# Kernel tuning notes

Hardware: AMD Instinct MI355X
Metric: run time of the kernel (lower is better)

## Reference

```python
import jax, jax.numpy as jnp
import numpy as np

T, B, E = 512, 128, 256  # timesteps, batch_size, embedding_size


def setup_inputs() -> dict:
    key = jax.random.key(0)
    k1, k2, k3 = jax.random.split(key, 3)
    return {
        "v": jax.random.normal(k1, (T, B, E), dtype=jnp.float32),
        "u": jax.random.uniform(k2, (T, B), dtype=jnp.float32),  # pop signals in (0,1)
        "d": jax.random.uniform(k3, (T, B), dtype=jnp.float32),  # push signals in (0,1)
    }


def _pop(s, w):
    """Grefenstette-stack pop: s [T,B] strengths (stack grows along dim 0,
    padded with zeros past the current depth), w [B] pop amount.
    Reverse cumsum, subtract w, clamp at 0, then difference to recover per-slot
    strengths. Zero padding at the tail is preserved exactly (contributes 0)."""
    top = jnp.cumsum(s[::-1], axis=0) - w[None, :]
    top = jnp.clip(top, 0.0)
    top = top - jnp.concatenate([jnp.zeros_like(top[:1]), top[:-1]], axis=0)
    return top[::-1]


def reference(v, u, d):
    # v: [T, B, E] pushed vectors; u, d: [T, B] pop/push strengths.
    T_, B_ = u.shape
    E_ = v.shape[-1]
    ones = jnp.ones((B_,), v.dtype)

    def step(carry, xs):
        V, s = carry  # V: [T,B,E] value buffer, s: [T,B] strengths (zero-padded)
        t, v_t, u_t, d_t = xs
        V = V.at[t].set(v_t)
        # forward(): pop with u (original detaches s and u inside pop), then push d
        s = _pop(jax.lax.stop_gradient(s), jax.lax.stop_gradient(u_t)).at[t].set(d_t)
        # read(): weights = s - pop(s, 1); r = sum_t weights * V
        weights = s - _pop(jax.lax.stop_gradient(s), ones)
        r = jnp.einsum('tb,tbe->be', weights, V)
        return (V, s), r

    init = (jnp.zeros((T_, B_, E_), v.dtype), jnp.zeros((T_, B_), v.dtype))
    _, rs = jax.lax.scan(step, init, (jnp.arange(T_), v, u, d))
    return rs  # [T, B, E] read vector at each timestep
```

## Files before the change

kernel.cpp:

```cpp
#include <hip/hip_runtime.h>

#define T_DIM 512
#define B_DIM 128
#define E_DIM 256
#define NEG_INF (-1e30f)

typedef float vfloat4 __attribute__((ext_vector_type(4)));


struct Node { float g; int ngl; };

__global__ void __launch_bounds__(512) scan_prep(
    const float* __restrict__ u, const float* __restrict__ d,
    float* __restrict__ S_out, Node* __restrict__ nodes)
{
    const int b    = blockIdx.x;
    const int t    = threadIdx.x;
    const int lane = t & 63;
    const int w    = t >> 6;

    __shared__ float wsum[8];
    __shared__ float wpre[8];
    __shared__ float M[10][T_DIM];

    const float dv = d[t * B_DIM + b];
    float x = dv - u[t * B_DIM + b];

    #pragma unroll
    for (int off = 1; off < 64; off <<= 1) {
        float y = __shfl_up(x, off, 64);
        if (lane >= off) x += y;
    }
    if (lane == 63) wsum[w] = x;
    __syncthreads();
    if (t < 8) {
        float s = 0.f;
        for (int i = 0; i < t; ++i) s += wsum[i];
        wpre[t] = s;
    }
    __syncthreads();
    const float S = x + wpre[w];
    const float g = dv - S;

    M[0][t] = g;
    __syncthreads();
    #pragma unroll
    for (int k = 1; k < 10; ++k) {
        int h = 1 << (k - 1);
        float left = (t >= h) ? M[k - 1][t - h] : NEG_INF;
        float mk = fmaxf(M[k - 1][t], left);
        __syncthreads();
        M[k][t] = mk;
        __syncthreads();
    }

    int m = t - 1;
    #pragma unroll
    for (int k = 9; k >= 0; --k) {
        if (m >= 0 && M[k][m] <= g) m -= (1 << k);
    }
    if (m < 0) m = -1;

    S_out[(b << 9) | t] = S;
    nodes[(b << 9) | t] = Node{g, m};
}

#define CPW 4
__global__ void __launch_bounds__(256) stack_read(
    const float* __restrict__ v, const float* __restrict__ S_in,
    const Node* __restrict__ nodes, float* __restrict__ out)
{
    const int wid  = (blockIdx.x << 2) | (threadIdx.x >> 6);
    const int lane = threadIdx.x & 63;
    const int e4   = lane << 2;

    float4 acc[CPW];
    float  prev[CPW], Sv[CPW];
    int    m[CPW], bb[CPW];
    bool   act[CPW];

    #pragma unroll
    for (int c = 0; c < CPW; ++c) {
        const int id = (wid << 2) | c;
        bb[c]  = id >> 9;
        m[c]   = id & 511;
        Sv[c]  = S_in[id];
        acc[c] = make_float4(0.f, 0.f, 0.f, 0.f);
        prev[c] = 0.f;
        act[c]  = true;
    }

    while (act[0] || act[1] || act[2] || act[3]) {
        Node  nd[CPW];
        float4 vv[CPW];
        #pragma unroll
        for (int c = 0; c < CPW; ++c) {
            if (act[c]) {
                nd[c] = nodes[(bb[c] << 9) | m[c]];
                vv[c] = *(const float4*)(v + ((size_t)m[c] * B_DIM + bb[c]) * E_DIM + e4);
            }
        }
        #pragma unroll
        for (int c = 0; c < CPW; ++c) {
            if (act[c]) {
                const float rc  = Sv[c] + nd[c].g;
                const float cur = fminf(rc, 1.f);
                const float wt  = cur - prev[c];
                acc[c].x += wt * vv[c].x;
                acc[c].y += wt * vv[c].y;
                acc[c].z += wt * vv[c].z;
                acc[c].w += wt * vv[c].w;
                prev[c] = cur;
                if (rc >= 1.f || nd[c].ngl < 0) act[c] = false;
                else                            m[c] = nd[c].ngl;
            }
        }
    }

    #pragma unroll
    for (int c = 0; c < CPW; ++c) {
        const int id = (wid << 2) | c;
        vfloat4 val = {acc[c].x, acc[c].y, acc[c].z, acc[c].w};
        vfloat4* o = (vfloat4*)(out + ((size_t)(id & 511) * B_DIM + (id >> 9)) * E_DIM + e4);
        __builtin_nontemporal_store(val, o);
    }
}

extern "C" void kernel_launch(void* const* d_in, const int* in_sizes, int n_in,
                              void* d_out, int out_size, void* d_ws, size_t ws_size,
                              hipStream_t stream) {
    const float* v = (const float*)d_in[0];
    const float* u = (const float*)d_in[1];
    const float* d = (const float*)d_in[2];
    float* out = (float*)d_out;

    float* S    = (float*)d_ws;
    Node*  node = (Node*)((char*)d_ws + (size_t)B_DIM * T_DIM * 4);

    scan_prep<<<dim3(B_DIM), 512, 0, stream>>>(u, d, S, node);
    stack_read<<<dim3((T_DIM * B_DIM) / (CPW * 4)), 256, 0, stream>>>(v, S, node, out);
}
```

Before: 137.8 us.

## Stage per-batch time windows of v in LDS and share chain walks

Each block now handles a 32-timestep window for one batch element. It loads that window's v rows, nodes and S into shared memory, plus up to 16 earlier chain rows found by walking back from the window start. Per-timestep read chains are then served from LDS first and fall back to global memory only past the cached prefix. This aims to cut redundant global gathers of the same v rows across neighbouring timesteps. The cost is extra shared memory, a serial single-lane prefix walk, and less parallel latency hiding than the previous 4-chain interleave.

```diff
diff --git a/kernel.cpp b/kernel.cpp
--- a/kernel.cpp
+++ b/kernel.cpp
@@ -4,6 +4,8 @@
 #define B_DIM 128
 #define E_DIM 256
 #define NEG_INF (-1e30f)
+#define W_WIN 32
+#define L_SLOTS 16
 
 typedef float vfloat4 __attribute__((ext_vector_type(4)));
 
@@ -65,64 +67,119 @@
     nodes[(b << 9) | t] = Node{g, m};
 }
 
-#define CPW 4
 __global__ void __launch_bounds__(256) stack_read(
     const float* __restrict__ v, const float* __restrict__ S_in,
     const Node* __restrict__ nodes, float* __restrict__ out)
 {
-    const int wid  = (blockIdx.x << 2) | (threadIdx.x >> 6);
-    const int lane = threadIdx.x & 63;
-    const int e4   = lane << 2;
+    __shared__ float vwin[W_WIN][E_DIM];
+    __shared__ float vL[L_SLOTS][E_DIM];
+    __shared__ float wg_g[W_WIN];
+    __shared__ int   wg_ngl[W_WIN];
+    __shared__ float wg_S[W_WIN];
+    __shared__ int   Lidx[L_SLOTS];
+    __shared__ float Lg[L_SLOTS];
+    __shared__ int   Lcount, Lnext;
 
-    float4 acc[CPW];
-    float  prev[CPW], Sv[CPW];
-    int    m[CPW], bb[CPW];
-    bool   act[CPW];
+    const int b     = blockIdx.x >> 4;
+    const int t0    = (blockIdx.x & 15) << 5;
+    const int tid   = threadIdx.x;
+    const int w     = tid >> 6;
+    const int lane  = tid & 63;
+    const int e4    = lane << 2;
+    const int nbase = b << 9;
 
-    #pragma unroll
-    for (int c = 0; c < CPW; ++c) {
-        const int id = (wid << 2) | c;
-        bb[c]  = id >> 9;
-        m[c]   = id & 511;
-        Sv[c]  = S_in[id];
-        acc[c] = make_float4(0.f, 0.f, 0.f, 0.f);
-        prev[c] = 0.f;
-        act[c]  = true;
+    if (w == 0) {
+        float sv = 1e30f;
+        if (lane < W_WIN) {
+            const int t = t0 + lane;
+            sv = S_in[nbase | t];
+            const Node nd = nodes[nbase | t];
+            wg_S[lane]   = sv;
+            wg_g[lane]   = nd.g;
+            wg_ngl[lane] = nd.ngl;
+        }
+        #pragma unroll
+        for (int off = 32; off; off >>= 1) sv = fminf(sv, __shfl_xor(sv, off, 64));
+        if (lane == 0) {
+            const float smin = sv;
+            int lc = 0, m = t0 - 1, mn = -1;
+            while (m >= 0 && lc < L_SLOTS) {
+                const Node nd = nodes[nbase | m];
+                Lidx[lc] = m; Lg[lc] = nd.g; ++lc;
+                mn = nd.ngl;
+                if (nd.g >= 1.0f - smin) break;
+                m = nd.ngl;
+            }
+            Lcount = lc; Lnext = mn;
+        }
     }
+    for (int r = w; r < W_WIN; r += 4) {
+        const float4 x = *(const float4*)(v + ((size_t)(t0 + r) * B_DIM + b) * E_DIM + e4);
+        *(float4*)&vwin[r][e4] = x;
+    }
+    __syncthreads();
+    const int lc = Lcount;
+    for (int r = w; r < lc; r += 4) {
+        const int m = Lidx[r];
+        const float4 x = *(const float4*)(v + ((size_t)m * B_DIM + b) * E_DIM + e4);
+        *(float4*)&vL[r][e4] = x;
+    }
+    __syncthreads();
+    const int lnx = Lnext;
 
-    while (act[0] || act[1] || act[2] || act[3]) {
-        Node  nd[CPW];
-        float4 vv[CPW];
-        #pragma unroll
-        for (int c = 0; c < CPW; ++c) {
-            if (act[c]) {
-                nd[c] = nodes[(bb[c] << 9) | m[c]];
-                vv[c] = *(const float4*)(v + ((size_t)m[c] * B_DIM + bb[c]) * E_DIM + e4);
+    for (int j = 0; j < 8; ++j) {
+        const int tw = (w << 3) | j;
+        const int t  = t0 + tw;
+        const float S = wg_S[tw];
+        float4 acc = make_float4(0.f, 0.f, 0.f, 0.f);
+        float prev = 0.f;
+        int m = t;
+        bool active = true;
+
+        while (active && m >= t0) {
+            const int k = m - t0;
+            const float g  = wg_g[k];
+            const float rc = S + g;
+            const float cur = fminf(rc, 1.f);
+            const float wt  = cur - prev; prev = cur;
+            const float4 vv = *(const float4*)&vwin[k][e4];
+            acc.x += wt * vv.x; acc.y += wt * vv.y;
+            acc.z += wt * vv.z; acc.w += wt * vv.w;
+            if (rc >= 1.f) { active = false; break; }
+            m = wg_ngl[k];
+            if (m < 0) active = false;
+        }
+        if (active && m >= 0) {
+            int i = 0;
+            while (i < lc && Lidx[i] != m) ++i;
+            if (i < lc) {
+                for (; i < lc; ++i) {
+                    const float g  = Lg[i];
+                    const float rc = S + g;
+                    const float cur = fminf(rc, 1.f);
+                    const float wt  = cur - prev; prev = cur;
+                    const float4 vv = *(const float4*)&vL[i][e4];
+                    acc.x += wt * vv.x; acc.y += wt * vv.y;
+                    acc.z += wt * vv.z; acc.w += wt * vv.w;
+                    if (rc >= 1.f) { active = false; break; }
+                }
+                if (active) m = lnx;
+            }
+            while (active && m >= 0) {
+                const Node nd = nodes[nbase | m];
+                const float rc = S + nd.g;
+                const float cur = fminf(rc, 1.f);
+                const float wt  = cur - prev; prev = cur;
+                const float4 vv = *(const float4*)(v + ((size_t)m * B_DIM + b) * E_DIM + e4);
+                acc.x += wt * vv.x; acc.y += wt * vv.y;
+                acc.z += wt * vv.z; acc.w += wt * vv.w;
+                if (rc >= 1.f) break;
+                m = nd.ngl;
             }
         }
-        #pragma unroll
-        for (int c = 0; c < CPW; ++c) {
-            if (act[c]) {
-                const float rc  = Sv[c] + nd[c].g;
-                const float cur = fminf(rc, 1.f);
-                const float wt  = cur - prev[c];
-                acc[c].x += wt * vv[c].x;
-                acc[c].y += wt * vv[c].y;
-                acc[c].z += wt * vv[c].z;
-                acc[c].w += wt * vv[c].w;
-                prev[c] = cur;
-                if (rc >= 1.f || nd[c].ngl < 0) act[c] = false;
-                else                            m[c] = nd[c].ngl;
-            }
-        }
-    }
-
-    #pragma unroll
-    for (int c = 0; c < CPW; ++c) {
-        const int id = (wid << 2) | c;
-        vfloat4 val = {acc[c].x, acc[c].y, acc[c].z, acc[c].w};
-        vfloat4* o = (vfloat4*)(out + ((size_t)(id & 511) * B_DIM + (id >> 9)) * E_DIM + e4);
-        __builtin_nontemporal_store(val, o);
+        const vfloat4 val = {acc.x, acc.y, acc.z, acc.w};
+        __builtin_nontemporal_store(val,
+            (vfloat4*)(out + ((size_t)t * B_DIM + b) * E_DIM + e4));
     }
 }
 
@@ -138,5 +195,5 @@
     Node*  node = (Node*)((char*)d_ws + (size_t)B_DIM * T_DIM * 4);
 
     scan_prep<<<dim3(B_DIM), 512, 0, stream>>>(u, d, S, node);
-    stack_read<<<dim3((T_DIM * B_DIM) / (CPW * 4)), 256, 0, stream>>>(v, S, node, out);
+    stack_read<<<dim3((T_DIM / W_WIN) * B_DIM), 256, 0, stream>>>(v, S, node, out);
 }
```

Result: slower. 151.4 us (+9.9%).

## Precompute per-query gather lists in scan kernel and batch independent vector loads

Applied to the files above, without the earlier changes.

The scan kernel now walks each query's chain of stack slots, capped at a fixed length, and writes the weights and slot indices into a per-query list in workspace. The read kernel reads these lists in chunks of four and issues four independent vector loads per chunk, instead of a dependent pointer-chase through node records for every step. Chains longer than the cap fall back to the old traversal. The change also swizzles block order and gives each wave two queries instead of four. In exchange it adds 256 bytes of list storage per query and moves serial chain walking into the prep kernel, which runs with only one block per batch element.

```diff
diff --git a/kernel.cpp b/kernel.cpp
--- a/kernel.cpp
+++ b/kernel.cpp
@@ -4,15 +4,17 @@
 #define B_DIM 128
 #define E_DIM 256
 #define NEG_INF (-1e30f)
+#define CAP 28
 
 typedef float vfloat4 __attribute__((ext_vector_type(4)));
 
 
 struct Node { float g; int ngl; };
 
+
 __global__ void __launch_bounds__(512) scan_prep(
     const float* __restrict__ u, const float* __restrict__ d,
-    float* __restrict__ S_out, Node* __restrict__ nodes)
+    float* __restrict__ lists, Node* __restrict__ nodes)
 {
     const int b    = blockIdx.x;
     const int t    = threadIdx.x;
@@ -22,6 +24,7 @@
     __shared__ float wsum[8];
     __shared__ float wpre[8];
     __shared__ float M[10][T_DIM];
+    __shared__ int   sngl[T_DIM];
 
     const float dv = d[t * B_DIM + b];
     float x = dv - u[t * B_DIM + b];
@@ -61,68 +64,101 @@
     }
     if (m < 0) m = -1;
 
-    S_out[(b << 9) | t] = S;
-    nodes[(b << 9) | t] = Node{g, m};
+    const int id = (b << 9) | t;
+    nodes[id] = Node{g, m};
+    sngl[t] = m;
+    __syncthreads();
+
+    float* Lb = lists + (size_t)id * 64;
+    float prev = 0.f;
+    int   cm = t, cnt = 0, cont_m = -1;
+    float cont_prev = 0.f;
+    while (true) {
+        const float gm = M[0][cm];
+        const float rc = S + gm;
+        const float cur = fminf(rc, 1.f);
+        Lb[4 + 2 * cnt] = cur - prev;
+        Lb[5 + 2 * cnt] = __int_as_float(cm);
+        prev = cur;
+        ++cnt;
+        if (rc >= 1.f) break;
+        const int nm = sngl[cm];
+        if (nm < 0) break;
+        cm = nm;
+        if (cnt == CAP) { cont_m = cm; cont_prev = prev; break; }
+    }
+    const int last_m = cm;
+    while (cnt & 3) {
+        Lb[4 + 2 * cnt] = 0.f;
+        Lb[5 + 2 * cnt] = __int_as_float(last_m);
+        ++cnt;
+    }
+    Lb[0] = __int_as_float(cnt);
+    Lb[1] = __int_as_float(cont_m);
+    Lb[2] = cont_prev;
+    Lb[3] = S;
 }
 
-#define CPW 4
-__global__ void __launch_bounds__(256) stack_read(
-    const float* __restrict__ v, const float* __restrict__ S_in,
+__global__ void __launch_bounds__(256) gather_read(
+    const float* __restrict__ v, const float* __restrict__ lists,
     const Node* __restrict__ nodes, float* __restrict__ out)
 {
-    const int wid  = (blockIdx.x << 2) | (threadIdx.x >> 6);
+    const int bid  = blockIdx.x;
+    const int swz  = ((bid & 7) << 10) | (bid >> 3);
+    const int wid  = (swz << 2) | (threadIdx.x >> 6);
     const int lane = threadIdx.x & 63;
     const int e4   = lane << 2;
 
-    float4 acc[CPW];
-    float  prev[CPW], Sv[CPW];
-    int    m[CPW], bb[CPW];
-    bool   act[CPW];
+    #pragma unroll
+    for (int c = 0; c < 2; ++c) {
+        const int id = (wid << 1) | c;
+        const int b  = id >> 9, t = id & 511;
+        const float* __restrict__ vb = v + (size_t)b * E_DIM + e4;
+        const float4* __restrict__ Lb = (const float4*)(lists + (size_t)id * 64);
 
-    #pragma unroll
-    for (int c = 0; c < CPW; ++c) {
-        const int id = (wid << 2) | c;
-        bb[c]  = id >> 9;
-        m[c]   = id & 511;
-        Sv[c]  = S_in[id];
-        acc[c] = make_float4(0.f, 0.f, 0.f, 0.f);
-        prev[c] = 0.f;
-        act[c]  = true;
-    }
+        const float4 hdr = Lb[0];
+        const int cnt    = __float_as_int(hdr.x);
+        const int cont_m = __float_as_int(hdr.y);
+        const int nch    = cnt >> 2;
 
-    while (act[0] || act[1] || act[2] || act[3]) {
-        Node  nd[CPW];
-        float4 vv[CPW];
-        #pragma unroll
-        for (int c = 0; c < CPW; ++c) {
-            if (act[c]) {
-                nd[c] = nodes[(bb[c] << 9) | m[c]];
-                vv[c] = *(const float4*)(v + ((size_t)m[c] * B_DIM + bb[c]) * E_DIM + e4);
+        float4 acc = make_float4(0.f, 0.f, 0.f, 0.f);
+        for (int ch = 0; ch < nch; ++ch) {
+            const float4 q0 = Lb[1 + 2 * ch];
+            const float4 q1 = Lb[2 + 2 * ch];
+            const int ma = __float_as_int(q0.y);
+            const int mb = __float_as_int(q0.w);
+            const int mc = __float_as_int(q1.y);
+            const int md = __float_as_int(q1.w);
+            const float4 va = *(const float4*)(vb + ((size_t)ma << 15));
+            const float4 vc2 = *(const float4*)(vb + ((size_t)mb << 15));
+            const float4 vc3 = *(const float4*)(vb + ((size_t)mc << 15));
+            const float4 vc4 = *(const float4*)(vb + ((size_t)md << 15));
+            acc.x += q0.x * va.x + q0.z * vc2.x + q1.x * vc3.x + q1.z * vc4.x;
+            acc.y += q0.x * va.y + q0.z * vc2.y + q1.x * vc3.y + q1.z * vc4.y;
+            acc.z += q0.x * va.z + q0.z * vc2.z + q1.x * vc3.z + q1.z * vc4.z;
+            acc.w += q0.x * va.w + q0.z * vc2.w + q1.x * vc3.w + q1.z * vc4.w;
+        }
+
+        if (cont_m >= 0) {
+            float prev = hdr.z;
+            const float S = hdr.w;
+            int m = cont_m;
+            while (m >= 0) {
+                const Node nd = nodes[(b << 9) | m];
+                const float rc = S + nd.g;
+                const float cur = fminf(rc, 1.f);
+                const float wt = cur - prev; prev = cur;
+                const float4 vv = *(const float4*)(vb + ((size_t)m << 15));
+                acc.x += wt * vv.x; acc.y += wt * vv.y;
+                acc.z += wt * vv.z; acc.w += wt * vv.w;
+                if (rc >= 1.f) break;
+                m = nd.ngl;
             }
         }
-        #pragma unroll
-        for (int c = 0; c < CPW; ++c) {
-            if (act[c]) {
-                const float rc  = Sv[c] + nd[c].g;
-                const float cur = fminf(rc, 1.f);
-                const float wt  = cur - prev[c];
-                acc[c].x += wt * vv[c].x;
-                acc[c].y += wt * vv[c].y;
-                acc[c].z += wt * vv[c].z;
-                acc[c].w += wt * vv[c].w;
-                prev[c] = cur;
-                if (rc >= 1.f || nd[c].ngl < 0) act[c] = false;
-                else                            m[c] = nd[c].ngl;
-            }
-        }
-    }
 
-    #pragma unroll
-    for (int c = 0; c < CPW; ++c) {
-        const int id = (wid << 2) | c;
-        vfloat4 val = {acc[c].x, acc[c].y, acc[c].z, acc[c].w};
-        vfloat4* o = (vfloat4*)(out + ((size_t)(id & 511) * B_DIM + (id >> 9)) * E_DIM + e4);
-        __builtin_nontemporal_store(val, o);
+        const vfloat4 val = {acc.x, acc.y, acc.z, acc.w};
+        __builtin_nontemporal_store(val,
+            (vfloat4*)(out + ((size_t)t * B_DIM + b) * E_DIM + e4));
     }
 }
 
@@ -134,9 +170,9 @@
     const float* d = (const float*)d_in[2];
     float* out = (float*)d_out;
 
-    float* S    = (float*)d_ws;
-    Node*  node = (Node*)((char*)d_ws + (size_t)B_DIM * T_DIM * 4);
+    Node*  node  = (Node*)d_ws;
+    float* lists = (float*)((char*)d_ws + ((size_t)1 << 20));
 
-    scan_prep<<<dim3(B_DIM), 512, 0, stream>>>(u, d, S, node);
-    stack_read<<<dim3((T_DIM * B_DIM) / (CPW * 4)), 256, 0, stream>>>(v, S, node, out);
+    scan_prep<<<dim3(B_DIM), 512, 0, stream>>>(u, d, lists, node);
+    gather_read<<<dim3((T_DIM * B_DIM) / 8), 256, 0, stream>>>(v, lists, node, out);
 }
```

New measurement: 141.7 us. 2.8% more time.

## Share chain traversal across 8 consecutive timesteps per wave with LDS-cached nodes

Applied to the files above, without the earlier changes.

Each wave now handles 8 consecutive timesteps of one batch column rather than 4 unrelated ones. They walk a merged greater-previous chain, so every loaded v row is reused across all 8 outputs, and a running max threshold decides which outputs take each element. The batch's node table is staged into shared memory and block ids are swizzled for locality. This aims to cut redundant global loads of v and of the nodes, in exchange for more per-element compare logic and a shared-memory staging step.

```diff
diff --git a/kernel.cpp b/kernel.cpp
--- a/kernel.cpp
+++ b/kernel.cpp
@@ -4,6 +4,8 @@
 #define B_DIM 128
 #define E_DIM 256
 #define NEG_INF (-1e30f)
+#define W 8
+#define DONE 1e30f
 
 typedef float vfloat4 __attribute__((ext_vector_type(4)));
 
@@ -65,64 +67,109 @@
     nodes[(b << 9) | t] = Node{g, m};
 }
 
-#define CPW 4
 __global__ void __launch_bounds__(256) stack_read(
     const float* __restrict__ v, const float* __restrict__ S_in,
     const Node* __restrict__ nodes, float* __restrict__ out)
 {
-    const int wid  = (blockIdx.x << 2) | (threadIdx.x >> 6);
+    __shared__ float2 snode[T_DIM];
+
+    const int bid = blockIdx.x;
+    const int swz = ((bid & 7) << 8) | (bid >> 3);
+    const int base_id = swz << 5;
+    const int b    = base_id >> 9;
+    const int wv   = threadIdx.x >> 6;
     const int lane = threadIdx.x & 63;
     const int e4   = lane << 2;
 
-    float4 acc[CPW];
-    float  prev[CPW], Sv[CPW];
-    int    m[CPW], bb[CPW];
-    bool   act[CPW];
+    {
+        const int i = threadIdx.x;
+        const Node n0 = nodes[(b << 9) | i];
+        const Node n1 = nodes[(b << 9) | (i + 256)];
+        snode[i]       = make_float2(n0.g, __int_as_float(n0.ngl));
+        snode[i + 256] = make_float2(n1.g, __int_as_float(n1.ngl));
+    }
+    __syncthreads();
+
+    const int tw = (base_id & 511) | (wv << 3);
+    const float* __restrict__ vb = v + (size_t)b * E_DIM + e4;
+
+    float4 acc[W];
+    float  M[W], prev[W], S[W];
+    #pragma unroll
+    for (int j = 0; j < W; ++j) {
+        acc[j] = make_float4(0.f, 0.f, 0.f, 0.f);
+        M[j] = NEG_INF; prev[j] = 0.f;
+        S[j] = S_in[base_id + (wv << 3) + j];
+    }
 
     #pragma unroll
-    for (int c = 0; c < CPW; ++c) {
-        const int id = (wid << 2) | c;
-        bb[c]  = id >> 9;
-        m[c]   = id & 511;
-        Sv[c]  = S_in[id];
-        acc[c] = make_float4(0.f, 0.f, 0.f, 0.f);
-        prev[c] = 0.f;
-        act[c]  = true;
+    for (int k = W - 1; k >= 0; --k) {
+        const int m = tw + k;
+        const float2 nd = snode[m];
+        const float g = nd.x;
+        const float4 vv = *(const float4*)(vb + ((size_t)m << 15));
+        #pragma unroll
+        for (int j = 0; j < W; ++j) {
+            if (j >= k) {
+                if (g > M[j]) {
+                    const float rc  = S[j] + g;
+                    const float cur = fminf(rc, 1.f);
+                    const float wt  = cur - prev[j];
+                    acc[j].x += wt * vv.x; acc[j].y += wt * vv.y;
+                    acc[j].z += wt * vv.z; acc[j].w += wt * vv.w;
+                    prev[j] = cur;
+                    M[j] = (rc >= 1.f) ? DONE : g;
+                }
+            }
+        }
     }
 
-    while (act[0] || act[1] || act[2] || act[3]) {
-        Node  nd[CPW];
-        float4 vv[CPW];
-        #pragma unroll
-        for (int c = 0; c < CPW; ++c) {
-            if (act[c]) {
-                nd[c] = nodes[(bb[c] << 9) | m[c]];
-                vv[c] = *(const float4*)(v + ((size_t)m[c] * B_DIM + bb[c]) * E_DIM + e4);
+    float thr = M[0];
+    #pragma unroll
+    for (int j = 1; j < W; ++j) thr = fminf(thr, M[j]);
+
+    if (thr < 1e29f) {
+        int p = __float_as_int(snode[tw].y);
+        while (p >= 0) {
+            const float2 nd = snode[p];
+            if (nd.x > thr) break;
+            p = __float_as_int(nd.y);
+        }
+        while (p >= 0) {
+            const float2 nd = snode[p];
+            const float g = nd.x;
+            const float4 vv = *(const float4*)(vb + ((size_t)p << 15));
+            #pragma unroll
+            for (int j = 0; j < W; ++j) {
+                if (g > M[j]) {
+                    const float rc  = S[j] + g;
+                    const float cur = fminf(rc, 1.f);
+                    const float wt  = cur - prev[j];
+                    acc[j].x += wt * vv.x; acc[j].y += wt * vv.y;
+                    acc[j].z += wt * vv.z; acc[j].w += wt * vv.w;
+                    prev[j] = cur;
+                    M[j] = (rc >= 1.f) ? DONE : g;
+                }
             }
-        }
-        #pragma unroll
-        for (int c = 0; c < CPW; ++c) {
-            if (act[c]) {
-                const float rc  = Sv[c] + nd[c].g;
-                const float cur = fminf(rc, 1.f);
-                const float wt  = cur - prev[c];
-                acc[c].x += wt * vv[c].x;
-                acc[c].y += wt * vv[c].y;
-                acc[c].z += wt * vv[c].z;
-                acc[c].w += wt * vv[c].w;
-                prev[c] = cur;
-                if (rc >= 1.f || nd[c].ngl < 0) act[c] = false;
-                else                            m[c] = nd[c].ngl;
+            thr = M[0];
+            #pragma unroll
+            for (int j = 1; j < W; ++j) thr = fminf(thr, M[j]);
+            if (thr > 1e29f) break;
+            p = __float_as_int(nd.y);
+            while (p >= 0) {
+                const float2 nd2 = snode[p];
+                if (nd2.x > thr) break;
+                p = __float_as_int(nd2.y);
             }
         }
     }
 
     #pragma unroll
-    for (int c = 0; c < CPW; ++c) {
-        const int id = (wid << 2) | c;
-        vfloat4 val = {acc[c].x, acc[c].y, acc[c].z, acc[c].w};
-        vfloat4* o = (vfloat4*)(out + ((size_t)(id & 511) * B_DIM + (id >> 9)) * E_DIM + e4);
-        __builtin_nontemporal_store(val, o);
+    for (int j = 0; j < W; ++j) {
+        const int t = tw + j;
+        const vfloat4 o = {acc[j].x, acc[j].y, acc[j].z, acc[j].w};
+        __builtin_nontemporal_store(o,
+            (vfloat4*)(out + ((size_t)t * B_DIM + b) * E_DIM + e4));
     }
 }
 
@@ -138,5 +185,5 @@
     Node*  node = (Node*)((char*)d_ws + (size_t)B_DIM * T_DIM * 4);
 
     scan_prep<<<dim3(B_DIM), 512, 0, stream>>>(u, d, S, node);
-    stack_read<<<dim3((T_DIM * B_DIM) / (CPW * 4)), 256, 0, stream>>>(v, S, node, out);
+    stack_read<<<dim3((T_DIM * B_DIM) / 32), 256, 0, stream>>>(v, S, node, out);
 }
```

Result: faster. 127.5 us, median of 2 (-7.5%).
